# Optimization experiments

Measured on AMD Instinct MI355X. Metric: run time of the kernel, lower is better.

## Reference

```python
import jax, jax.numpy as jnp
import numpy as np

SEQ = 4096
EMBED = 1280
HEADS = 16
HEAD_DIM = EMBED // HEADS  # 80


def rotate_half(x):
    # interleaved rotate: out[..., 2i] = -x[..., 2i+1]; out[..., 2i+1] = x[..., 2i]
    x_even = x[..., ::2]
    x_odd = x[..., 1::2]
    return jnp.stack((-x_odd, x_even), axis=-1).reshape(x.shape)


def setup_inputs() -> dict:
    key = jax.random.key(0)
    ks = jax.random.split(key, 7)
    return {
        "hidden_states": jax.random.normal(ks[0], (SEQ, EMBED), dtype=jnp.float32),
        "cos": jax.random.uniform(ks[1], (SEQ, HEAD_DIM), dtype=jnp.float32),
        "sin": jax.random.uniform(ks[2], (SEQ, HEAD_DIM), dtype=jnp.float32),
        "w_qkv": jax.random.normal(ks[3], (EMBED, 3 * EMBED), dtype=jnp.float32) * 0.02,
        "b_qkv": jax.random.normal(ks[4], (3 * EMBED,), dtype=jnp.float32) * 0.02,
        "w_proj": jax.random.normal(ks[5], (EMBED, EMBED), dtype=jnp.float32) * 0.02,
        "b_proj": jax.random.normal(ks[6], (EMBED,), dtype=jnp.float32) * 0.02,
    }


def reference(hidden_states, cos, sin, w_qkv, b_qkv, w_proj, b_proj):
    S = hidden_states.shape[0]
    # QKV projection: (S, 3E) -> (S, 3, H, D)
    qkv = (hidden_states @ w_qkv + b_qkv).reshape(S, 3, HEADS, HEAD_DIM)
    q, k, v = qkv[:, 0], qkv[:, 1], qkv[:, 2]  # each (S, H, D)

    # RoPE in float32, cos/sin broadcast over heads: (S, 1, D)
    dt = q.dtype
    qf, kf = q.astype(jnp.float32), k.astype(jnp.float32)
    c = cos[:, None, :].astype(jnp.float32)
    s = sin[:, None, :].astype(jnp.float32)
    q = (qf * c + rotate_half(qf) * s).astype(dt)
    k = (kf * c + rotate_half(kf) * s).astype(dt)

    scaling = HEAD_DIM ** -0.5
    # attention scores per head: (H, S, S)
    scores = jnp.einsum("shd,thd->hst", q, k) * scaling
    attn = jax.nn.softmax(scores.astype(jnp.float32), axis=-1).astype(dt)
    # weighted values: (S, H, D)
    out = jnp.einsum("hst,thd->shd", attn, v).reshape(S, EMBED)
    return out @ w_proj + b_proj
```

## Files before the change

### kernel.cpp

```cpp
#include <hip/hip_runtime.h>
#include <hip/hip_bf16.h>

#define SEQ   4096
#define EMBED 1280
#define NH    16
#define HD    80
#define K1    EMBED
#define N1    (3*EMBED)

typedef short bfrag_t __attribute__((ext_vector_type(8)));
typedef float f32x4   __attribute__((ext_vector_type(4)));
typedef float f32x16  __attribute__((ext_vector_type(16)));

static __device__ __forceinline__ unsigned short f2bf(float x){
    __hip_bfloat16 h = __float2bfloat16(x);
    return __builtin_bit_cast(unsigned short, h);
}
static __device__ __forceinline__ float bf2f(unsigned short u){
    unsigned int v = ((unsigned int)u) << 16;
    return __builtin_bit_cast(float, v);
}

static __device__ __forceinline__ unsigned int pack2bf(float a, float b){
#if __has_builtin(__builtin_amdgcn_cvt_pk_bf16_f32)
    short2 p = __builtin_amdgcn_cvt_pk_bf16_f32(a, b);
    return __builtin_bit_cast(unsigned int, p);
#else
    unsigned int ua = __builtin_bit_cast(unsigned int, a) + 0x8000u;
    unsigned int ub = __builtin_bit_cast(unsigned int, b) + 0x8000u;
#if __has_builtin(__builtin_amdgcn_perm)
    return __builtin_amdgcn_perm(ub, ua, 0x07060302u);
#else
    return (ua >> 16) | (ub & 0xFFFF0000u);
#endif
#endif
}

static __device__ __forceinline__ float fast_exp2(float x){
#if __has_builtin(__builtin_amdgcn_exp2f)
    return __builtin_amdgcn_exp2f(x);
#else
    return __expf(x * 0.69314718056f);
#endif
}

static __device__ __forceinline__ void gload_lds16(const void* g, void* l){
#if __has_builtin(__builtin_amdgcn_global_load_lds)
    __builtin_amdgcn_global_load_lds(
        (const __attribute__((address_space(1))) unsigned int*)g,
        (__attribute__((address_space(3))) unsigned int*)l, 16, 0, 0);
#else
    *(uint4*)l = *(const uint4*)g;
#endif
}

static __device__ __forceinline__ bfrag_t ld_frag8(const unsigned short* p){
    uint2 lo = *(const uint2*)p;
    uint2 hi = *(const uint2*)(p + 4);
    uint4 u; u.x = lo.x; u.y = lo.y; u.z = hi.x; u.w = hi.y;
    return __builtin_bit_cast(bfrag_t, u);
}

#define CONV_BLOCKS (SEQ*EMBED/4/256)
#define TQ_BX (N1/32)
#define TQ_BLOCKS (TQ_BX*(K1/32))
#define TP_BX (EMBED/32)
#define TP_BLOCKS (TP_BX*(EMBED/32))

__global__ __launch_bounds__(256)
void prep_all(const float* __restrict__ hs, unsigned short* __restrict__ hb,
              const float* __restrict__ wqkv, unsigned short* __restrict__ wqT,
              const float* __restrict__ wproj, unsigned short* __restrict__ wpT)
{
    __shared__ float t[32][33];
    int b = blockIdx.x;
    if (b < CONV_BLOCKS){
        int i = b * 256 + threadIdx.x;
        float4 v = ((const float4*)hs)[i];
        ushort4 r;
        r.x = f2bf(v.x); r.y = f2bf(v.y); r.z = f2bf(v.z); r.w = f2bf(v.w);
        ((ushort4*)hb)[i] = r;
        return;
    }
    const float* in; unsigned short* outp; int R, C, bc, br;
    if (b < CONV_BLOCKS + TQ_BLOCKS){
        b -= CONV_BLOCKS;
        in = wqkv; outp = wqT; R = K1; C = N1;
        bc = (b % TQ_BX) * 32; br = (b / TQ_BX) * 32;
    } else {
        b -= CONV_BLOCKS + TQ_BLOCKS;
        in = wproj; outp = wpT; R = EMBED; C = EMBED;
        bc = (b % TP_BX) * 32; br = (b / TP_BX) * 32;
    }
    int tx = threadIdx.x & 31, ty = threadIdx.x >> 5;
    for (int i = ty; i < 32; i += 8) t[i][tx] = in[(size_t)(br + i) * C + bc + tx];
    __syncthreads();
    for (int i = ty; i < 32; i += 8) outp[(size_t)(bc + i) * R + br + tx] = f2bf(t[tx][i]);
}


__global__ __launch_bounds__(256, 4)
void gemm_qkv(const unsigned short* __restrict__ A,
              const unsigned short* __restrict__ BT,
              const float* __restrict__ bias,
              const float* __restrict__ cosp, const float* __restrict__ sinp,
              unsigned short* __restrict__ qout, unsigned short* __restrict__ kout,
              unsigned short* __restrict__ vout,
              int M, int N, int K)
{
    __shared__ union {
        struct { unsigned short A[128*64]; unsigned short B[128*64]; } ab;
        unsigned short tr[4][64][72];
    } lds;

    int tid  = threadIdx.x;
    int lane = tid & 63, wave = tid >> 6;
    int wm = wave >> 1, wn = wave & 1;
    int quad = lane >> 4, l16 = lane & 15;
    int m0 = blockIdx.y * 128, n0 = blockIdx.x * 128;

    const unsigned short* pa[4];
    const unsigned short* pb[4];
    int dsto[4];
    #pragma unroll
    for (int rnd = 0; rnd < 4; rnd++){
        int idx = rnd*256 + tid;
        int row = idx >> 3, c = idx & 7;
        int cc = (c ^ (row & 7)) * 8;
        pa[rnd] = A  + (size_t)(m0 + row) * K + cc;
        pb[rnd] = BT + (size_t)(n0 + row) * K + cc;
        dsto[rnd] = idx * 8;
    }

    f32x4 acc[4][4] = {};

    for (int k0 = 0; k0 < K; k0 += 64){
        __syncthreads();
        #pragma unroll
        for (int rnd = 0; rnd < 4; rnd++){
            gload_lds16(pa[rnd], &lds.ab.A[dsto[rnd]]);
            gload_lds16(pb[rnd], &lds.ab.B[dsto[rnd]]);
            pa[rnd] += 64; pb[rnd] += 64;
        }
        __syncthreads();
        #pragma unroll
        for (int kk = 0; kk < 2; kk++){
            bfrag_t af[4], bf[4];
            #pragma unroll
            for (int i = 0; i < 4; i++){
                int row = wm*64 + i*16 + l16;
                af[i] = *(const bfrag_t*)&lds.ab.A[row*64 + (((kk*4+quad) ^ (l16 & 7)) << 3)];
            }
            #pragma unroll
            for (int j = 0; j < 4; j++){
                int row = wn*64 + j*16 + l16;
                bf[j] = *(const bfrag_t*)&lds.ab.B[row*64 + (((kk*4+quad) ^ (l16 & 7)) << 3)];
            }
            #pragma unroll
            for (int i = 0; i < 4; i++)
                #pragma unroll
                for (int j = 0; j < 4; j++)
                    acc[i][j] = __builtin_amdgcn_mfma_f32_16x16x32_bf16(af[i], bf[j], acc[i][j], 0, 0, 0);
        }
    }

    const float scaling = 0.11180339887498949f;

    if (n0 >= 2*EMBED){
        __syncthreads();
        #pragma unroll
        for (int j = 0; j < 4; j++){
            int colw = j*16 + l16;
            float b = bias[n0 + wn*64 + colw];
            #pragma unroll
            for (int i = 0; i < 4; i++){
                ushort4 u;
                u.x = f2bf(acc[i][j][0] + b);
                u.y = f2bf(acc[i][j][1] + b);
                u.z = f2bf(acc[i][j][2] + b);
                u.w = f2bf(acc[i][j][3] + b);
                *(ushort4*)&lds.tr[wave][colw][i*16 + quad*4] = u;
            }
        }
        int c8 = lane >> 3, rc = lane & 7;
        #pragma unroll
        for (int cg = 0; cg < 8; cg++){
            int colw = cg*8 + c8;
            size_t colg = (size_t)(n0 - 2*EMBED) + wn*64 + colw;
            int rowg = m0 + wm*64 + rc*8;
            *(uint4*)&vout[colg*SEQ + rowg] = *(const uint4*)&lds.tr[wave][colw][rc*8];
        }
        return;
    }

    #pragma unroll
    for (int i = 0; i < 4; i++)
    #pragma unroll
    for (int j = 0; j < 4; j++){
        int colj  = n0 + wn*64 + j*16;
        int which = colj / EMBED;
        int rem   = colj - which*EMBED;
        int hh    = rem / HD;
        int dd    = rem - hh*HD;
        float b = bias[colj + l16];
        unsigned short* dst = (which == 0) ? qout : kout;
        float mult = (which == 0) ? scaling : 1.f;
        #pragma unroll
        for (int r = 0; r < 4; r++){
            int row = m0 + wm*64 + i*16 + quad*4 + r;
            float v = acc[i][j][r] + b;
            float vo = __shfl_xor(v, 1, 64);
            float c = cosp[(size_t)row*HD + dd + l16];
            float s = sinp[(size_t)row*HD + dd + l16];
            float o = (l16 & 1) ? (v*c + vo*s) : (v*c - vo*s);
            dst[((size_t)hh*SEQ + row)*HD + dd + l16] = f2bf(o * mult);
        }
    }
}


__global__ __launch_bounds__(256, 4)
void gemm_proj(const unsigned short* __restrict__ A,
               const unsigned short* __restrict__ BT,
               const float* __restrict__ bias,
               float* __restrict__ out,
               int M, int N, int K)
{
    __shared__ unsigned short As[64*32];
    __shared__ unsigned short Bs[128*32];
    int tid  = threadIdx.x;
    int lane = tid & 63, wave = tid >> 6;
    int wm = wave & 1, wn = wave >> 1;
    int quad = lane >> 4, l16 = lane & 15;
    int m0 = blockIdx.y * 64, n0 = blockIdx.x * 128;

    f32x4 acc[2][4] = {};
    const unsigned short* ga = A  + (size_t)(m0 + (tid>>2)) * K + (tid&3)*8;
    const unsigned short* gb = BT + (size_t)(n0 + (tid>>2)) * K + (tid&3)*8;

    for (int k0 = 0; k0 < K; k0 += 32){
        __syncthreads();
        gload_lds16(ga,                &As[tid*8]);
        gload_lds16(gb,                &Bs[tid*8]);
        gload_lds16(gb + (size_t)64*K, &Bs[2048 + tid*8]);
        ga += 32; gb += 32;
        __syncthreads();
        bfrag_t af[2], bf[4];
        #pragma unroll
        for (int i = 0; i < 2; i++)
            af[i] = *(const bfrag_t*)&As[(wm*32 + i*16 + l16)*32 + quad*8];
        #pragma unroll
        for (int j = 0; j < 4; j++)
            bf[j] = *(const bfrag_t*)&Bs[(wn*64 + j*16 + l16)*32 + quad*8];
        #pragma unroll
        for (int i = 0; i < 2; i++)
            #pragma unroll
            for (int j = 0; j < 4; j++)
                acc[i][j] = __builtin_amdgcn_mfma_f32_16x16x32_bf16(af[i], bf[j], acc[i][j], 0, 0, 0);
    }

    #pragma unroll
    for (int i = 0; i < 2; i++)
    #pragma unroll
    for (int j = 0; j < 4; j++){
        int col = n0 + wn*64 + j*16 + l16;
        float b = bias[col];
        #pragma unroll
        for (int r = 0; r < 4; r++){
            int row = m0 + wm*32 + i*16 + quad*4 + r;
            out[(size_t)row * N + col] = acc[i][j][r] + b;
        }
    }
}


__global__ __launch_bounds__(256, 4)
void attn_mfma(const unsigned short* __restrict__ q,
               const unsigned short* __restrict__ k,
               const unsigned short* __restrict__ vt,
               unsigned short* __restrict__ out,
               unsigned short* __restrict__ opart,
               float* __restrict__ lpart,
               int iters)
{
    __shared__ unsigned short Vt[2][80*64];
    __shared__ unsigned short Ps[128][68];

    int tid  = threadIdx.x;
    int lane = tid & 63, wave = tid >> 6;
    int quad = lane >> 4, l16 = lane & 15;
    int l32  = lane & 31, h2 = lane >> 5;
    int h = blockIdx.y, q0 = blockIdx.x * 128;
    int split = blockIdx.z;
    int kb0 = split * iters * 64;
    int qrow = wave*32 + l32;

    const unsigned short* qh = q  + ((size_t)h*SEQ + q0)*HD;
    const unsigned short* kh = k  + (size_t)h*SEQ*HD;
    const unsigned short* vh = vt + (size_t)h*HD*SEQ;

    bfrag_t qf[5];
    #pragma unroll
    for (int kk = 0; kk < 5; kk++)
        qf[kk] = *(const bfrag_t*)&qh[(size_t)qrow*HD + (kk*2 + h2)*8];

    auto stage = [&](int buf, int kb){
        unsigned short* dst = &Vt[buf][0];
        #pragma unroll
        for (int rnd = 0; rnd < 3; rnd++){
            int idx = rnd*256 + tid;
            if (rnd < 2 || tid < 128){
                int row = idx >> 3, c = idx & 7;
                gload_lds16(&vh[(size_t)row*SEQ + kb + ((c ^ (row & 7)) << 3)], &dst[idx*8]);
            }
        }
    };

    stage(0, kb0);

    float la = 0.f, lb = 0.f;
    f32x4 o_[2][5] = {};

    const unsigned short* kp = kh + (size_t)(kb0 + l32)*HD + h2*8;
    const float LOG2E = 1.44269504f;
    const float BIAS2 = -17.3123405f;

    for (int kt = 0; kt < iters; kt++){
        f32x16 S0 = {}, S1 = {};
        #pragma unroll
        for (int kk = 0; kk < 5; kk++){
            bfrag_t kf0 = *(const bfrag_t*)(kp + kk*16);
            bfrag_t kf1 = *(const bfrag_t*)(kp + (size_t)32*HD + kk*16);
            S0 = __builtin_amdgcn_mfma_f32_32x32x16_bf16(kf0, qf[kk], S0, 0,0,0);
            S1 = __builtin_amdgcn_mfma_f32_32x32x16_bf16(kf1, qf[kk], S1, 0,0,0);
        }
        kp += (size_t)64*HD;

        #pragma unroll
        for (int r = 0; r < 16; r++){
            float p0 = fast_exp2(fmaf(S0[r], LOG2E, BIAS2));
            float p1 = fast_exp2(fmaf(S1[r], LOG2E, BIAS2));
            S0[r] = p0; S1[r] = p1;
            la += p0; lb += p1;
        }

        #pragma unroll
        for (int g = 0; g < 4; g++){
            uint2 w0, w1;
            w0.x = pack2bf(S0[g*4+0], S0[g*4+1]);
            w0.y = pack2bf(S0[g*4+2], S0[g*4+3]);
            w1.x = pack2bf(S1[g*4+0], S1[g*4+1]);
            w1.y = pack2bf(S1[g*4+2], S1[g*4+3]);
            *(uint2*)&Ps[qrow][g*8 + h2*4]      = w0;
            *(uint2*)&Ps[qrow][32 + g*8 + h2*4] = w1;
        }

        __syncthreads();
        if (kt + 1 < iters) stage((kt+1)&1, kb0 + (kt+1)*64);

        int buf = kt & 1;
        #pragma unroll
        for (int kk = 0; kk < 2; kk++){
            bfrag_t pf0 = ld_frag8(&Ps[wave*32      + l16][kk*32 + quad*8]);
            bfrag_t pf1 = ld_frag8(&Ps[wave*32 + 16 + l16][kk*32 + quad*8]);
            #pragma unroll
            for (int dt = 0; dt < 5; dt++){
                int row = dt*16 + l16;
                bfrag_t vf = *(const bfrag_t*)&Vt[buf][row*64 + (((kk*4+quad) ^ (l16 & 7)) << 3)];
                o_[0][dt] = __builtin_amdgcn_mfma_f32_16x16x32_bf16(vf, pf0, o_[0][dt], 0,0,0);
                o_[1][dt] = __builtin_amdgcn_mfma_f32_16x16x32_bf16(vf, pf1, o_[1][dt], 0,0,0);
            }
        }
    }

    float l_ = la + lb;
    l_ += __shfl_xor(l_, 32, 64);

    if (gridDim.z == 1){
        #pragma unroll
        for (int i = 0; i < 2; i++){
            float linv = 1.f / __shfl(l_, i*16 + l16, 64);
            int qg = q0 + wave*32 + i*16 + l16;
            #pragma unroll
            for (int dt = 0; dt < 5; dt++){
                int d = dt*16 + quad*4;
                ushort4 u;
                u.x = f2bf(o_[i][dt][0]*linv);
                u.y = f2bf(o_[i][dt][1]*linv);
                u.z = f2bf(o_[i][dt][2]*linv);
                u.w = f2bf(o_[i][dt][3]*linv);
                *(ushort4*)&out[(size_t)qg*EMBED + h*HD + d] = u;
            }
        }
    } else {
        if (h2 == 0)
            lpart[((size_t)(split*NH + h))*SEQ + q0 + qrow] = l_;
        #pragma unroll
        for (int i = 0; i < 2; i++){
            int qg = q0 + wave*32 + i*16 + l16;
            size_t base = (((size_t)(split*NH + h))*SEQ + qg)*HD;
            #pragma unroll
            for (int dt = 0; dt < 5; dt++){
                int d = dt*16 + quad*4;
                ushort4 u;
                u.x = f2bf(o_[i][dt][0]);
                u.y = f2bf(o_[i][dt][1]);
                u.z = f2bf(o_[i][dt][2]);
                u.w = f2bf(o_[i][dt][3]);
                *(ushort4*)&opart[base + d] = u;
            }
        }
    }
}

__global__ __launch_bounds__(256)
void attn_combine(const unsigned short* __restrict__ op,
                  const float* __restrict__ lp,
                  unsigned short* __restrict__ out,
                  int ns)
{
    int t = blockIdx.x*256 + threadIdx.x;
    int d8 = t % 10;
    int qh = t / 10;
    int q  = qh & (SEQ-1);
    int h  = qh >> 12;
    float lsum = 0.f;
    for (int s = 0; s < ns; s++) lsum += lp[((size_t)(s*NH + h))*SEQ + q];
    float inv = 1.f / lsum;
    float acc[8] = {};
    for (int s = 0; s < ns; s++){
        uint4 A = *(const uint4*)&op[(((size_t)(s*NH + h))*SEQ + q)*HD + d8*8];
        unsigned int* a = (unsigned int*)&A;
        #pragma unroll
        for (int e = 0; e < 4; e++){
            acc[2*e]   += bf2f((unsigned short)(a[e] & 0xffff));
            acc[2*e+1] += bf2f((unsigned short)(a[e] >> 16));
        }
    }
    uint4 R;
    unsigned int* r = (unsigned int*)&R;
    #pragma unroll
    for (int e = 0; e < 4; e++)
        r[e] = pack2bf(acc[2*e]*inv, acc[2*e+1]*inv);
    *(uint4*)&out[(size_t)q*EMBED + h*HD + d8*8] = R;
}


extern "C" void kernel_launch(void* const* d_in, const int* in_sizes, int n_in,
                              void* d_out, int out_size, void* d_ws, size_t ws_size,
                              hipStream_t stream)
{
    const float* hs    = (const float*)d_in[0];
    const float* cosp  = (const float*)d_in[1];
    const float* sinp  = (const float*)d_in[2];
    const float* wqkv  = (const float*)d_in[3];
    const float* bqkv  = (const float*)d_in[4];
    const float* wproj = (const float*)d_in[5];
    const float* bproj = (const float*)d_in[6];
    float* out = (float*)d_out;

    char* ws = (char*)d_ws;
    size_t off = 0;
    auto alloc = [&](size_t bytes){ void* p = ws + off; off += bytes; return p; };
    unsigned short* hb    = (unsigned short*)alloc((size_t)SEQ*EMBED*2);
    unsigned short* wqT   = (unsigned short*)alloc((size_t)N1*K1*2);
    unsigned short* wpT   = (unsigned short*)alloc((size_t)EMBED*EMBED*2);
    unsigned short* q_ws  = (unsigned short*)alloc((size_t)SEQ*EMBED*2);
    unsigned short* k_ws  = (unsigned short*)alloc((size_t)SEQ*EMBED*2);
    unsigned short* v_ws  = (unsigned short*)alloc((size_t)SEQ*EMBED*2);
    unsigned short* a_ws  = (unsigned short*)alloc((size_t)SEQ*EMBED*2);
    size_t base = off;
    size_t per_split = (size_t)NH*SEQ*HD*2 + (size_t)NH*SEQ*4;
    int nsplit = (ws_size >= base + 2*per_split) ? 2 : 1;
    unsigned short* opart = (unsigned short*)alloc((size_t)nsplit*NH*SEQ*HD*2);
    float*          lpart = (float*)alloc((size_t)nsplit*NH*SEQ*4);

    prep_all<<<CONV_BLOCKS + TQ_BLOCKS + TP_BLOCKS, 256, 0, stream>>>(
        hs, hb, wqkv, wqT, wproj, wpT);

    gemm_qkv<<<dim3(N1/128, SEQ/128), 256, 0, stream>>>(
        hb, wqT, bqkv, cosp, sinp, q_ws, k_ws, v_ws, SEQ, N1, K1);

    attn_mfma<<<dim3(SEQ/128, NH, nsplit), 256, 0, stream>>>(
        q_ws, k_ws, v_ws, a_ws, opart, lpart, (SEQ/64)/nsplit);
    if (nsplit > 1)
        attn_combine<<<NH*SEQ*10/256, 256, 0, stream>>>(opart, lpart, a_ws, nsplit);

    gemm_proj<<<dim3(EMBED/128, SEQ/64), 256, 0, stream>>>(
        a_ws, wpT, bproj, out, SEQ, EMBED, EMBED);
}
```

Baseline: 303.0 us.

## Double K-tile depth in projection GEMM with XOR-swizzled LDS, remap attention block order

The output projection GEMM now stages a 64-wide K slice per iteration instead of 32. LDS columns are XOR-swizzled by row so fragment reads avoid bank conflicts, and the number of barriers per K step is halved. The attention kernel remaps its block index so that consecutive blocks cover different heads for the same query tile. This is meant to spread work and K/V reuse more evenly across caches. The cost is double the LDS footprint for the GEMM, which could lower occupancy.

```diff
diff --git a/kernel.cpp b/kernel.cpp
--- a/kernel.cpp
+++ b/kernel.cpp
@@ -226,37 +226,57 @@
                float* __restrict__ out,
                int M, int N, int K)
 {
-    __shared__ unsigned short As[64*32];
-    __shared__ unsigned short Bs[128*32];
+    __shared__ unsigned short As[64*64];
+    __shared__ unsigned short Bs[128*64];
     int tid  = threadIdx.x;
     int lane = tid & 63, wave = tid >> 6;
     int wm = wave & 1, wn = wave >> 1;
     int quad = lane >> 4, l16 = lane & 15;
     int m0 = blockIdx.y * 64, n0 = blockIdx.x * 128;
 
+    const unsigned short* pa[2];
+    const unsigned short* pb[4];
+    int da[2], db[4];
+    #pragma unroll
+    for (int rnd = 0; rnd < 2; rnd++){
+        int idx = rnd*256 + tid;
+        int row = idx >> 3, c = idx & 7;
+        pa[rnd] = A + (size_t)(m0 + row) * K + ((c ^ (row & 7)) * 8);
+        da[rnd] = idx * 8;
+    }
+    #pragma unroll
+    for (int rnd = 0; rnd < 4; rnd++){
+        int idx = rnd*256 + tid;
+        int row = idx >> 3, c = idx & 7;
+        pb[rnd] = BT + (size_t)(n0 + row) * K + ((c ^ (row & 7)) * 8);
+        db[rnd] = idx * 8;
+    }
+
     f32x4 acc[2][4] = {};
-    const unsigned short* ga = A  + (size_t)(m0 + (tid>>2)) * K + (tid&3)*8;
-    const unsigned short* gb = BT + (size_t)(n0 + (tid>>2)) * K + (tid&3)*8;
-
-    for (int k0 = 0; k0 < K; k0 += 32){
+
+    for (int k0 = 0; k0 < K; k0 += 64){
         __syncthreads();
-        gload_lds16(ga,                &As[tid*8]);
-        gload_lds16(gb,                &Bs[tid*8]);
-        gload_lds16(gb + (size_t)64*K, &Bs[2048 + tid*8]);
-        ga += 32; gb += 32;
+        #pragma unroll
+        for (int rnd = 0; rnd < 2; rnd++){ gload_lds16(pa[rnd], &As[da[rnd]]); pa[rnd] += 64; }
+        #pragma unroll
+        for (int rnd = 0; rnd < 4; rnd++){ gload_lds16(pb[rnd], &Bs[db[rnd]]); pb[rnd] += 64; }
         __syncthreads();
-        bfrag_t af[2], bf[4];
-        #pragma unroll
-        for (int i = 0; i < 2; i++)
-            af[i] = *(const bfrag_t*)&As[(wm*32 + i*16 + l16)*32 + quad*8];
-        #pragma unroll
-        for (int j = 0; j < 4; j++)
-            bf[j] = *(const bfrag_t*)&Bs[(wn*64 + j*16 + l16)*32 + quad*8];
-        #pragma unroll
-        for (int i = 0; i < 2; i++)
+        #pragma unroll
+        for (int kk = 0; kk < 2; kk++){
+            int ch = ((kk*4+quad) ^ (l16 & 7)) << 3;
+            bfrag_t af[2], bf[4];
+            #pragma unroll
+            for (int i = 0; i < 2; i++)
+                af[i] = *(const bfrag_t*)&As[(wm*32 + i*16 + l16)*64 + ch];
             #pragma unroll
             for (int j = 0; j < 4; j++)
-                acc[i][j] = __builtin_amdgcn_mfma_f32_16x16x32_bf16(af[i], bf[j], acc[i][j], 0, 0, 0);
+                bf[j] = *(const bfrag_t*)&Bs[(wn*64 + j*16 + l16)*64 + ch];
+            #pragma unroll
+            for (int i = 0; i < 2; i++)
+                #pragma unroll
+                for (int j = 0; j < 4; j++)
+                    acc[i][j] = __builtin_amdgcn_mfma_f32_16x16x32_bf16(af[i], bf[j], acc[i][j], 0, 0, 0);
+        }
     }
 
     #pragma unroll
@@ -290,7 +310,9 @@
     int lane = tid & 63, wave = tid >> 6;
     int quad = lane >> 4, l16 = lane & 15;
     int l32  = lane & 31, h2 = lane >> 5;
-    int h = blockIdx.y, q0 = blockIdx.x * 128;
+    int lin = blockIdx.y * (SEQ/128) + blockIdx.x;
+    int h  = lin & (NH-1);
+    int q0 = (lin >> 4) * 128;
     int split = blockIdx.z;
     int kb0 = split * iters * 64;
     int qrow = wave*32 + l32;
```

Result: slower. 309.1 us (+2.0%).
